# Optimization experiments

Measured on AMD Instinct MI355X. Metric: run time of the kernel, lower is better.

Reference implementation:

```python
import jax, jax.numpy as jnp
import numpy as np

B = 131072
D = 256
N_SC = 16
SC_CAP = 2
MAX_USERS = 8
POW_DIM = 10


def setup_inputs() -> dict:
    key = jax.random.key(0)
    k0, k1, k2, k3 = jax.random.split(key, 4)
    x = jax.random.normal(k0, (B, D), dtype=jnp.float32)
    available_actions = jax.random.randint(k1, (B, 2 * MAX_USERS), 0, 2).astype(jnp.int32)
    # per-head Categorical weights: Linear(D, action_dim), small init (gain=0.01 orthogonal-ish)
    W_sc = jax.random.normal(k2, (MAX_USERS, D, N_SC), dtype=jnp.float32) * 0.01
    b_sc = jnp.zeros((MAX_USERS, N_SC), dtype=jnp.float32)
    W_pow = jax.random.normal(k3, (MAX_USERS, D, POW_DIM), dtype=jnp.float32) * 0.01
    b_pow = jnp.zeros((MAX_USERS, POW_DIM), dtype=jnp.float32)
    return {"x": x, "available_actions": available_actions,
            "W_sc": W_sc, "b_sc": b_sc, "W_pow": W_pow, "b_pow": b_pow}


def reference(x, available_actions, W_sc, b_sc, W_pow, b_pow):
    # NOMA branch of MultiDiscreteACTLayer.forward (deterministic=False).
    Bn = x.shape[0]
    key = jax.random.key(42)
    sc_keys = jax.random.split(key, MAX_USERS)
    pow_key = jax.random.fold_in(key, 999)

    NEG = jnp.float32(-1e10)

    def sc_step(sc_stat, inp):
        W, b, avail, k = inp  # W:[D,N_SC], b:[N_SC], avail:[Bn] float, k: key
        logits = x @ W + b                       # [Bn, N_SC]
        mask = sc_stat < SC_CAP                  # subchannel still has capacity
        logits = jnp.where(mask, logits, NEG)
        action = jax.random.categorical(k, logits)        # [Bn] int
        logp = jnp.take_along_axis(jax.nn.log_softmax(logits, -1),
                                   action[:, None], axis=-1)[:, 0]
        # availability masking: unavailable -> action=-1, logp=0
        action = jnp.where(avail > 0, action, -1)
        logp = logp * avail
        # scatter: sc_stat[b, action] += 1 where action != -1
        upd = jnp.where((action >= 0)[:, None],
                        jax.nn.one_hot(jnp.maximum(action, 0), N_SC, dtype=sc_stat.dtype),
                        jnp.zeros((), sc_stat.dtype))
        return sc_stat + upd, (action, logp)

    sc_stat0 = jnp.zeros((Bn, N_SC), dtype=x.dtype)
    avail_f = available_actions.astype(x.dtype)
    avail_sc = avail_f[:, :MAX_USERS].T          # [MAX_USERS, Bn]
    _, (sc_actions, sc_logps) = jax.lax.scan(
        sc_step, sc_stat0, (W_sc, b_sc, avail_sc, sc_keys))

    # power heads: no mask, no loop-carried state -> fully batched
    pow_logits = jnp.einsum('bd,hdk->bhk', x, W_pow) + b_pow   # [Bn, H, POW_DIM]
    pow_actions = jax.random.categorical(pow_key, pow_logits)  # [Bn, H]
    pow_logps = jnp.take_along_axis(jax.nn.log_softmax(pow_logits, -1),
                                    pow_actions[..., None], axis=-1)[..., 0]
    avail_pow = avail_f[:, MAX_USERS:]
    pow_actions = jnp.where(avail_pow > 0, pow_actions, -1)
    pow_logps = pow_logps * avail_pow

    actions = jnp.concatenate([sc_actions.T, pow_actions], axis=-1)          # [Bn, 16]
    action_log_probs = jnp.concatenate([sc_logps.T, pow_logps], axis=-1)
    action_log_probs = jnp.sum(action_log_probs, axis=-1, keepdims=True)     # [Bn, 1]
    return actions, action_log_probs, available_actions
```

## Files before the change

### kernel.cpp

```cpp
#include <hip/hip_runtime.h>


#define B_TOTAL 131072
#define NCOL    208
#define ROWS    32
#define TINYF   1.17549435e-38f
#define THRF    2.0e-3f

#define WPLANE  53248
#define XB_L    8448
#define XB_P    264
#define LGP     36

typedef float f32x4 __attribute__((ext_vector_type(4)));
typedef short short8 __attribute__((ext_vector_type(8)));

#define MFMA_BF16(A,B,C) __builtin_amdgcn_mfma_f32_16x16x32_bf16((A),(B),(C),0,0,0)

#define ROR16(v, n) __uint_as_float((unsigned)__builtin_amdgcn_update_dpp(     \
    (int)__float_as_uint(v), (int)__float_as_uint(v), 0x120 | (n), 0xF, 0xF, false))

__device__ __forceinline__ float redmax16(float v) {
  v = fmaxf(v, ROR16(v, 8));
  v = fmaxf(v, ROR16(v, 4));
  v = fmaxf(v, ROR16(v, 2));
  v = fmaxf(v, ROR16(v, 1));
  return v;
}
__device__ __forceinline__ float redsum16(float v) {
  v += ROR16(v, 8);
  v += ROR16(v, 4);
  v += ROR16(v, 2);
  v += ROR16(v, 1);
  return v;
}

struct TF2 { unsigned a, b; };

__host__ __device__ constexpr unsigned rotl_(unsigned x, int r) {
  return (x << r) | (x >> (32 - r));
}

__host__ __device__ constexpr TF2 tf2(unsigned k0, unsigned k1, unsigned x0, unsigned x1) {
  unsigned ks0 = k0, ks1 = k1, ks2 = k0 ^ k1 ^ 0x1BD11BDAu;
  x0 += ks0; x1 += ks1;
  x0 += x1; x1 = rotl_(x1, 13); x1 ^= x0;
  x0 += x1; x1 = rotl_(x1, 15); x1 ^= x0;
  x0 += x1; x1 = rotl_(x1, 26); x1 ^= x0;
  x0 += x1; x1 = rotl_(x1,  6); x1 ^= x0;
  x0 += ks1; x1 += ks2 + 1u;
  x0 += x1; x1 = rotl_(x1, 17); x1 ^= x0;
  x0 += x1; x1 = rotl_(x1, 29); x1 ^= x0;
  x0 += x1; x1 = rotl_(x1, 16); x1 ^= x0;
  x0 += x1; x1 = rotl_(x1, 24); x1 ^= x0;
  x0 += ks2; x1 += ks0 + 2u;
  x0 += x1; x1 = rotl_(x1, 13); x1 ^= x0;
  x0 += x1; x1 = rotl_(x1, 15); x1 ^= x0;
  x0 += x1; x1 = rotl_(x1, 26); x1 ^= x0;
  x0 += x1; x1 = rotl_(x1,  6); x1 ^= x0;
  x0 += ks0; x1 += ks1 + 3u;
  x0 += x1; x1 = rotl_(x1, 17); x1 ^= x0;
  x0 += x1; x1 = rotl_(x1, 29); x1 ^= x0;
  x0 += x1; x1 = rotl_(x1, 16); x1 ^= x0;
  x0 += x1; x1 = rotl_(x1, 24); x1 ^= x0;
  x0 += ks1; x1 += ks2 + 4u;
  x0 += x1; x1 = rotl_(x1, 13); x1 ^= x0;
  x0 += x1; x1 = rotl_(x1, 15); x1 ^= x0;
  x0 += x1; x1 = rotl_(x1, 26); x1 ^= x0;
  x0 += x1; x1 = rotl_(x1,  6); x1 ^= x0;
  x0 += ks2; x1 += ks0 + 5u;
  return TF2{x0, x1};
}

__host__ __device__ constexpr unsigned key_a(unsigned d) { return tf2(0u, 42u, 0u, d).a; }
__host__ __device__ constexpr unsigned key_b(unsigned d) { return tf2(0u, 42u, 0u, d).b; }

constexpr unsigned SK0c[8] = {
  key_a(0), key_a(1), key_a(2), key_a(3), key_a(4), key_a(5), key_a(6), key_a(7)
};
constexpr unsigned SK1c[8] = {
  key_b(0), key_b(1), key_b(2), key_b(3), key_b(4), key_b(5), key_b(6), key_b(7)
};
constexpr unsigned PK0 = key_a(999);
constexpr unsigned PK1 = key_b(999);

__device__ __forceinline__ double dlog(double xd) {
  long long b = __double_as_longlong(xd);
  int e = (int)(b >> 52) - 1023;
  double m = __longlong_as_double((b & 0x000FFFFFFFFFFFFFLL) | 0x3FF0000000000000LL);
  if (m > 1.4142135623730951) { m *= 0.5; e += 1; }
  double mp1 = m + 1.0;
  double r = (double)__builtin_amdgcn_rcpf((float)mp1);
  r = fma(fma(-mp1, r, 1.0), r, r);
  double z  = (m - 1.0) * r;
  double z2 = z * z;
  double p = fma(z2, fma(z2, fma(z2, fma(z2, fma(z2,
              1.0/13.0, 1.0/11.0), 1.0/9.0), 1.0/7.0), 1.0/5.0), 1.0/3.0);
  double lm = fma(2.0 * z, z2 * p, 2.0 * z);
  return fma((double)e, 0.6931471805599453, lm);
}

__device__ __forceinline__ float gumbelf(unsigned bits) {
  float u = __uint_as_float((bits >> 9) | 0x3f800000u) - 1.0f;
  u = u + TINYF;
  u = fmaxf(TINYF, u);
  double nl = -dlog((double)u);
  return -(float)dlog(nl);
}

__device__ __attribute__((noinline)) float gumbel_precise(unsigned k0, unsigned k1,
                                                          unsigned cnt) {
  TF2 r = tf2(k0, k1, 0u, cnt);
  return gumbelf(r.a ^ r.b);
}

__device__ __forceinline__ float gumbel_fast(unsigned bits) {
  float u = __uint_as_float((bits >> 9) | 0x3f800000u) - 1.0f;
  u = fmaxf(TINYF, u + TINYF);
  float t = u - 1.0f;
  float q  = fmaf(t, 0.33333333f, -0.5f);
  float pl = -t * fmaf(t, q, 1.0f);
  float hw = -__logf(u);
  float nl = (t > -0.0078125f) ? pl : hw;
  return -__logf(nl);
}

__global__ void repack_kernel(const float* __restrict__ Wsc, const float* __restrict__ bsc,
                              const float* __restrict__ Wpow, const float* __restrict__ bpow,
                              short* __restrict__ Wb, float* __restrict__ bp) {
  int t = blockIdx.x * 256 + threadIdx.x;
  if (t < 53248) {
    int j    = t & 7;
    int lane = (t >> 3) & 63;
    int c    = (t >> 9) & 7;
    int T    = t >> 12;
    int k    = c * 32 + (lane >> 4) * 8 + j;
    int col  = T * 16 + (lane & 15);
    int u = col / 26, n = col % 26;
    float w = (n < 16) ? Wsc[(u * 256 + k) * 16 + n]
                       : Wpow[(u * 256 + k) * 10 + (n - 16)];
    unsigned b0 = __float_as_uint(w) & 0xFFFF0000u;
    float f1 = w - __uint_as_float(b0);
    unsigned b1 = __float_as_uint(f1) & 0xFFFF0000u;
    float f2 = f1 - __uint_as_float(b1);
    unsigned b2 = __float_as_uint(f2) & 0xFFFF0000u;
    int idx = (T * 8 + c) * 512 + lane * 8 + j;
    Wb[idx]              = (short)(b0 >> 16);
    Wb[WPLANE + idx]     = (short)(b1 >> 16);
    Wb[2 * WPLANE + idx] = (short)(b2 >> 16);
  } else {
    int cc = t - 53248;
    float v = 0.f;
    if (cc < NCOL) {
      int u = cc / 26, n = cc % 26;
      v = (n < 16) ? bsc[u * 16 + n] : bpow[u * 10 + (n - 16)];
    }
    bp[cc] = v;
  }
}

#define PROD8(X0, X1, X2, W0, W1, W2, AM, AS) do {                      \
    AM = MFMA_BF16(X0, W0, AM);                                         \
    AS = MFMA_BF16(X1, W0, AS);                                         \
    AS = MFMA_BF16(X0, W1, AS);                                         \
    AS = MFMA_BF16(X1, W1, AS);                                         \
    AS = MFMA_BF16(X2, W0, AS);                                         \
    AS = MFMA_BF16(X0, W2, AS);                                         \
    AS = MFMA_BF16(X2, W1, AS);                                         \
    AS = MFMA_BF16(X1, W2, AS);                                         \
  } while (0)

__global__ __launch_bounds__(512, 4) void act_kernel(
    const float* __restrict__ x, const int* __restrict__ avail,
    const short* __restrict__ Wb, const float* __restrict__ bp,
    float* __restrict__ out) {
  __shared__ __align__(16) union SMem {
    short xb[3][ROWS][XB_P];
    struct {
      float gpow[ROWS][80];
      float lgT[NCOL][LGP];
    } c;
  } sm;

  const int t = threadIdx.x;
  const int b0 = blockIdx.x * ROWS;

  const int av = avail[(size_t)(b0 + (t >> 4)) * 16 + (t & 15)];

#pragma unroll
  for (int i = 0; i < 4; ++i) {
    int flat = t + 512 * i;
    int r  = flat >> 6;
    int kq = flat & 63;
    float4 v = ((const float4*)(x + (size_t)(b0 + r) * 256))[kq];
    unsigned L0[4], L1[4], L2[4];
#pragma unroll
    for (int e = 0; e < 4; ++e) {
      float f = (&v.x)[e];
      unsigned h0 = __float_as_uint(f) & 0xFFFF0000u;
      float f1 = f - __uint_as_float(h0);
      unsigned h1 = __float_as_uint(f1) & 0xFFFF0000u;
      float f2 = f1 - __uint_as_float(h1);
      unsigned h2 = __float_as_uint(f2) & 0xFFFF0000u;
      L0[e] = h0; L1[e] = h1; L2[e] = h2;
    }
    int ks = 4 * kq;
    *(uint2*)&sm.xb[0][r][ks] =
        make_uint2((L0[0] >> 16) | (L0[1] & 0xFFFF0000u),
                   (L0[2] >> 16) | (L0[3] & 0xFFFF0000u));
    *(uint2*)&sm.xb[1][r][ks] =
        make_uint2((L1[0] >> 16) | (L1[1] & 0xFFFF0000u),
                   (L1[2] >> 16) | (L1[3] & 0xFFFF0000u));
    *(uint2*)&sm.xb[2][r][ks] =
        make_uint2((L2[0] >> 16) | (L2[1] & 0xFFFF0000u),
                   (L2[2] >> 16) | (L2[3] & 0xFFFF0000u));
  }
  __syncthreads();

  const int lane64 = t & 63;
  const int wv  = t >> 6;
  const int q   = lane64 >> 4;
  const int r16 = lane64 & 15;
  const int tA  = (wv + (blockIdx.x & 7)) & 7;
  const bool heavy = tA < 5;
  const int tB  = 8 + tA;

  const f32x4 fz = {0.f, 0.f, 0.f, 0.f};
  f32x4 dA0, dA1, dB0, dB1;
  int i0, jo;
  {
    f32x4 mA0 = fz, sA0 = fz, mA1 = fz, sA1 = fz;
    f32x4 mB0 = fz, sB0 = fz, mB1 = fz, sB1 = fz;

    const short* xr0 = &sm.xb[0][r16][0];
    const short* xr1 = &sm.xb[0][16 + r16][0];
    const int wlane = lane64 * 8;

#pragma unroll 1
    for (int c = 0; c < 8; ++c) {
      const int xo = c * 32 + q * 8;
      short8 a0 = *(const short8*)(xr0 + xo);
      short8 a1 = *(const short8*)(xr0 + XB_L + xo);
      short8 a2 = *(const short8*)(xr0 + 2 * XB_L + xo);
      short8 c0_ = *(const short8*)(xr1 + xo);
      short8 c1_ = *(const short8*)(xr1 + XB_L + xo);
      short8 c2_ = *(const short8*)(xr1 + 2 * XB_L + xo);
      {
        const int wi = (tA * 8 + c) * 512 + wlane;
        short8 w0 = *(const short8*)(Wb + wi);
        short8 w1 = *(const short8*)(Wb + WPLANE + wi);
        short8 w2 = *(const short8*)(Wb + 2 * WPLANE + wi);
        PROD8(a0,  a1,  a2,  w0, w1, w2, mA0, sA0);
        PROD8(c0_, c1_, c2_, w0, w1, w2, mA1, sA1);
      }
      if (heavy) {
        const int wi = (tB * 8 + c) * 512 + wlane;
        short8 w0 = *(const short8*)(Wb + wi);
        short8 w1 = *(const short8*)(Wb + WPLANE + wi);
        short8 w2 = *(const short8*)(Wb + 2 * WPLANE + wi);
        PROD8(a0,  a1,  a2,  w0, w1, w2, mB0, sB0);
        PROD8(c0_, c1_, c2_, w0, w1, w2, mB1, sB1);
      }
    }

    short8 pa = {0, 0, 0, 0, 0, 0, 0, 0};
    short8 pb = {0, 0, 0, 0, 0, 0, 0, 0};
    if (q == 0) {
      pa[0] = (short)(__float_as_uint((float)r16) >> 16);
      pb[0] = (short)0x3F80;
    }
    f32x4 pr = MFMA_BF16(pa, pb, fz);
    f32x4 pc = MFMA_BF16(pb, pa, fz);
    i0 = ((int)(pr[0] + 0.5f)) & 15;
    jo = ((int)(pc[0] + 0.5f)) & 15;

    dA0 = mA0 + sA0; dA1 = mA1 + sA1;
    dB0 = mB0 + sB0; dB1 = mB1 + sB1;
  }
  __syncthreads();

  {
    const int cA = tA * 16 + jo;
    float bpA = bp[cA];
    float4 v0, v1;
    v0.x = dA0[0] + bpA; v0.y = dA0[1] + bpA; v0.z = dA0[2] + bpA; v0.w = dA0[3] + bpA;
    v1.x = dA1[0] + bpA; v1.y = dA1[1] + bpA; v1.z = dA1[2] + bpA; v1.w = dA1[3] + bpA;
    *(float4*)&sm.c.lgT[cA][i0]      = v0;
    *(float4*)&sm.c.lgT[cA][16 + i0] = v1;
    if (heavy) {
      const int cB = tB * 16 + jo;
      float bpB = bp[cB];
      v0.x = dB0[0] + bpB; v0.y = dB0[1] + bpB; v0.z = dB0[2] + bpB; v0.w = dB0[3] + bpB;
      v1.x = dB1[0] + bpB; v1.y = dB1[1] + bpB; v1.z = dB1[2] + bpB; v1.w = dB1[3] + bpB;
      *(float4*)&sm.c.lgT[cB][i0]      = v0;
      *(float4*)&sm.c.lgT[cB][16 + i0] = v1;
    }
  }

#pragma unroll
  for (int i = 0; i < 5; ++i) {
    int flat = t + 512 * i;
    int prw  = (flat * 13108) >> 20;
    int q80  = flat - prw * 80;
    unsigned cnt = (unsigned)((b0 + prw) * 80 + q80);
    TF2 r = tf2(PK0, PK1, 0u, cnt);
    sm.c.gpow[prw][q80] = gumbel_fast(r.a ^ r.b);
  }

  float gsc[8];
  const unsigned cnt_sc = (unsigned)((b0 + (t >> 4)) * 16 + (t & 15));
#pragma unroll
  for (int u = 0; u < 8; ++u) {
    TF2 r = tf2(SK0c[u], SK1c[u], 0u, cnt_sc);
    gsc[u] = gumbel_fast(r.a ^ r.b);
  }
  __syncthreads();

  const int row  = t >> 4;
  const int lane = t & 15;
  const int g16  = (t & 63) >> 4;
  const int shamt = g16 * 16;
  const int gb   = b0 + row;
  const unsigned avm = (unsigned)((__ballot(av > 0) >> shamt) & 0xFFFFull);
  int stat = 0;
  float lpsum = 0.0f;
  float my_act = 0.0f;

#pragma unroll
  for (int u = 0; u < 8; ++u) {
    float logit = sm.c.lgT[u * 26 + lane][row];
    float ml = (stat < 2) ? logit : -1e10f;
    float y  = ml + gsc[u];
    float vmax = redmax16(y);
    unsigned bal = (unsigned)((__ballot(vmax - y < THRF) >> shamt) & 0xFFFFull);
    int idx;
    if (__builtin_popcount(bal) > 1) {
      float gp = gumbel_precise(SK0c[u], SK1c[u], cnt_sc);
      float yp = ml + gp;
      float vp = redmax16(yp);
      idx = __builtin_ctz((unsigned)((__ballot(yp == vp) >> shamt) & 0xFFFFull));
    } else {
      idx = __builtin_ctz(bal);
    }
    float s = redsum16(__expf(ml));
    float mlidx = redmax16((lane == idx) ? ml : -3.0e38f);
    float lp = mlidx - __logf(s);
    int au = (int)((avm >> u) & 1u);
    if (au) {
      lpsum += lp;
      if (lane == idx) stat += 1;
    }
    if (lane == u) my_act = au ? (float)idx : -1.0f;
  }

#pragma unroll
  for (int h = 0; h < 8; ++h) {
    bool on = lane < 10;
    float logit = on ? sm.c.lgT[h * 26 + 16 + lane][row] : -3.0e38f;
    float y     = on ? (logit + sm.c.gpow[row][h * 10 + lane]) : -3.0e38f;
    float vmax = redmax16(y);
    unsigned bal = (unsigned)((__ballot(vmax - y < THRF) >> shamt) & 0xFFFFull);
    int idx;
    if (__builtin_popcount(bal) > 1) {
      float gp = gumbel_precise(PK0, PK1, (unsigned)(gb * 80 + h * 10 + lane));
      float yp = on ? (logit + gp) : -3.0e38f;
      float vp = redmax16(yp);
      idx = __builtin_ctz((unsigned)((__ballot(yp == vp) >> shamt) & 0xFFFFull));
    } else {
      idx = __builtin_ctz(bal);
    }
    float s = redsum16(on ? __expf(logit) : 0.0f);
    float mlidx = redmax16((lane == idx) ? logit : -3.0e38f);
    float lp = mlidx - __logf(s);
    int ah = (int)((avm >> (8 + h)) & 1u);
    if (ah) lpsum += lp;
    if (lane == 8 + h) my_act = ah ? (float)idx : -1.0f;
  }

  out[(size_t)gb * 16 + lane] = my_act;
  if (lane == 0) out[(size_t)B_TOTAL * 16 + gb] = lpsum;
  out[(size_t)B_TOTAL * 17 + (size_t)gb * 16 + lane] = (float)av;
}

extern "C" void kernel_launch(void* const* d_in, const int* in_sizes, int n_in,
                              void* d_out, int out_size, void* d_ws, size_t ws_size,
                              hipStream_t stream) {
  const float* x    = (const float*)d_in[0];
  const int*   av   = (const int*)  d_in[1];
  const float* Wsc  = (const float*)d_in[2];
  const float* bsc  = (const float*)d_in[3];
  const float* Wpow = (const float*)d_in[4];
  const float* bpow = (const float*)d_in[5];
  float* outp = (float*)d_out;

  float* bp = (float*)d_ws;
  short* Wb = (short*)((char*)d_ws + 1024);

  repack_kernel<<<209, 256, 0, stream>>>(Wsc, bsc, Wpow, bpow, Wb, bp);
  act_kernel<<<B_TOTAL / ROWS, 512, 0, stream>>>(x, av, Wb, bp, outp);
}
```

Before: 361.8 us.

## Split fused kernel into GEMM and sampling kernels via global logits buffer

Splits the single fused kernel into a GEMM kernel that writes transposed logits to a workspace buffer and a separate sampling kernel that reads them back. The intent is to decouple the two phases so each gets its own block size and shared-memory footprint, improving occupancy. The cost is a large extra round trip of logits through global memory. The old fused kernel remains as a fallback when the workspace is too small.

```diff
diff --git a/kernel.cpp b/kernel.cpp
--- a/kernel.cpp
+++ b/kernel.cpp
@@ -170,6 +170,224 @@
     AS = MFMA_BF16(X1, W2, AS);                                         \
   } while (0)
 
+#define PHASE_A_BODY(XB, DA0, DA1, DB0, DB1, I0, JO)                          \
+  const int lane64 = t & 63;                                                  \
+  const int wv  = t >> 6;                                                     \
+  const int q   = lane64 >> 4;                                                \
+  const int r16 = lane64 & 15;                                                \
+  const int tA  = (wv + (blockIdx.x & 7)) & 7;                                \
+  const bool heavy = tA < 5;                                                  \
+  const int tB  = 8 + tA;                                                     \
+  const f32x4 fz = {0.f, 0.f, 0.f, 0.f};                                      \
+  {                                                                           \
+    f32x4 mA0 = fz, sA0 = fz, mA1 = fz, sA1 = fz;                             \
+    f32x4 mB0 = fz, sB0 = fz, mB1 = fz, sB1 = fz;                             \
+    const short* xr0 = &XB[0][r16][0];                                        \
+    const short* xr1 = &XB[0][16 + r16][0];                                   \
+    const int wlane = lane64 * 8;                                             \
+    _Pragma("unroll 1")                                                       \
+    for (int c = 0; c < 8; ++c) {                                             \
+      const int xo = c * 32 + q * 8;                                          \
+      short8 a0 = *(const short8*)(xr0 + xo);                                 \
+      short8 a1 = *(const short8*)(xr0 + XB_L + xo);                          \
+      short8 a2 = *(const short8*)(xr0 + 2 * XB_L + xo);                      \
+      short8 c0_ = *(const short8*)(xr1 + xo);                                \
+      short8 c1_ = *(const short8*)(xr1 + XB_L + xo);                         \
+      short8 c2_ = *(const short8*)(xr1 + 2 * XB_L + xo);                     \
+      {                                                                       \
+        const int wi = (tA * 8 + c) * 512 + wlane;                            \
+        short8 w0 = *(const short8*)(Wb + wi);                                \
+        short8 w1 = *(const short8*)(Wb + WPLANE + wi);                       \
+        short8 w2 = *(const short8*)(Wb + 2 * WPLANE + wi);                   \
+        PROD8(a0,  a1,  a2,  w0, w1, w2, mA0, sA0);                           \
+        PROD8(c0_, c1_, c2_, w0, w1, w2, mA1, sA1);                           \
+      }                                                                       \
+      if (heavy) {                                                            \
+        const int wi = (tB * 8 + c) * 512 + wlane;                            \
+        short8 w0 = *(const short8*)(Wb + wi);                                \
+        short8 w1 = *(const short8*)(Wb + WPLANE + wi);                       \
+        short8 w2 = *(const short8*)(Wb + 2 * WPLANE + wi);                   \
+        PROD8(a0,  a1,  a2,  w0, w1, w2, mB0, sB0);                           \
+        PROD8(c0_, c1_, c2_, w0, w1, w2, mB1, sB1);                           \
+      }                                                                       \
+    }                                                                         \
+    short8 pa = {0, 0, 0, 0, 0, 0, 0, 0};                                     \
+    short8 pb = {0, 0, 0, 0, 0, 0, 0, 0};                                     \
+    if (q == 0) {                                                             \
+      pa[0] = (short)(__float_as_uint((float)r16) >> 16);                     \
+      pb[0] = (short)0x3F80;                                                  \
+    }                                                                         \
+    f32x4 pr = MFMA_BF16(pa, pb, fz);                                         \
+    f32x4 pc = MFMA_BF16(pb, pa, fz);                                         \
+    I0 = ((int)(pr[0] + 0.5f)) & 15;                                          \
+    JO = ((int)(pc[0] + 0.5f)) & 15;                                          \
+    DA0 = mA0 + sA0; DA1 = mA1 + sA1;                                         \
+    DB0 = mB0 + sB0; DB1 = mB1 + sB1;                                         \
+  }
+
+#define STAGE_X(XB)                                                           \
+  _Pragma("unroll")                                                           \
+  for (int i = 0; i < 4; ++i) {                                               \
+    int flat = t + 512 * i;                                                   \
+    int r  = flat >> 6;                                                       \
+    int kq = flat & 63;                                                       \
+    float4 v = ((const float4*)(x + (size_t)(b0 + r) * 256))[kq];             \
+    unsigned L0[4], L1[4], L2[4];                                             \
+    _Pragma("unroll")                                                         \
+    for (int e = 0; e < 4; ++e) {                                             \
+      float f = (&v.x)[e];                                                    \
+      unsigned h0 = __float_as_uint(f) & 0xFFFF0000u;                         \
+      float f1 = f - __uint_as_float(h0);                                     \
+      unsigned h1 = __float_as_uint(f1) & 0xFFFF0000u;                        \
+      float f2 = f1 - __uint_as_float(h1);                                    \
+      unsigned h2 = __float_as_uint(f2) & 0xFFFF0000u;                        \
+      L0[e] = h0; L1[e] = h1; L2[e] = h2;                                     \
+    }                                                                         \
+    int ks = 4 * kq;                                                          \
+    *(uint2*)&XB[0][r][ks] =                                                  \
+        make_uint2((L0[0] >> 16) | (L0[1] & 0xFFFF0000u),                     \
+                   (L0[2] >> 16) | (L0[3] & 0xFFFF0000u));                    \
+    *(uint2*)&XB[1][r][ks] =                                                  \
+        make_uint2((L1[0] >> 16) | (L1[1] & 0xFFFF0000u),                     \
+                   (L1[2] >> 16) | (L1[3] & 0xFFFF0000u));                    \
+    *(uint2*)&XB[2][r][ks] =                                                  \
+        make_uint2((L2[0] >> 16) | (L2[1] & 0xFFFF0000u),                     \
+                   (L2[2] >> 16) | (L2[3] & 0xFFFF0000u));                    \
+  }
+
+__global__ __launch_bounds__(512, 4) void gemm_kernel(
+    const float* __restrict__ x, const short* __restrict__ Wb,
+    const float* __restrict__ bp, float* __restrict__ lgT) {
+  __shared__ __align__(16) short xb[3][ROWS][XB_P];
+  const int t = threadIdx.x;
+  const int b0 = blockIdx.x * ROWS;
+
+  STAGE_X(xb)
+  __syncthreads();
+
+  f32x4 dA0, dA1, dB0, dB1;
+  int i0, jo;
+  PHASE_A_BODY(xb, dA0, dA1, dB0, dB1, i0, jo)
+
+  {
+    const int cA = tA * 16 + jo;
+    float bpA = bp[cA];
+    float4 v0, v1;
+    v0.x = dA0[0] + bpA; v0.y = dA0[1] + bpA; v0.z = dA0[2] + bpA; v0.w = dA0[3] + bpA;
+    v1.x = dA1[0] + bpA; v1.y = dA1[1] + bpA; v1.z = dA1[2] + bpA; v1.w = dA1[3] + bpA;
+    float* base = lgT + (size_t)cA * B_TOTAL + b0;
+    *(float4*)(base + i0)      = v0;
+    *(float4*)(base + 16 + i0) = v1;
+    if (heavy) {
+      const int cB = tB * 16 + jo;
+      float bpB = bp[cB];
+      v0.x = dB0[0] + bpB; v0.y = dB0[1] + bpB; v0.z = dB0[2] + bpB; v0.w = dB0[3] + bpB;
+      v1.x = dB1[0] + bpB; v1.y = dB1[1] + bpB; v1.z = dB1[2] + bpB; v1.w = dB1[3] + bpB;
+      float* baseB = lgT + (size_t)cB * B_TOTAL + b0;
+      *(float4*)(baseB + i0)      = v0;
+      *(float4*)(baseB + 16 + i0) = v1;
+    }
+  }
+}
+
+__global__ __launch_bounds__(256, 4) void sample_kernel(
+    const float* __restrict__ lgT, const int* __restrict__ avail,
+    float* __restrict__ out) {
+  __shared__ float gpow[16][80];
+  const int t = threadIdx.x;
+  const int b0 = blockIdx.x * 16;
+  const int row  = t >> 4;
+  const int lane = t & 15;
+  const int gb   = b0 + row;
+  const int av = avail[(size_t)gb * 16 + lane];
+
+  float lsc[8];
+#pragma unroll
+  for (int u = 0; u < 8; ++u)
+    lsc[u] = lgT[(size_t)(u * 26 + lane) * B_TOTAL + gb];
+
+#pragma unroll
+  for (int i = 0; i < 5; ++i) {
+    int flat = t + 256 * i;
+    int prw  = (flat * 13108) >> 20;
+    int q80  = flat - prw * 80;
+    unsigned cnt = (unsigned)((b0 + prw) * 80 + q80);
+    TF2 r = tf2(PK0, PK1, 0u, cnt);
+    gpow[prw][q80] = gumbel_fast(r.a ^ r.b);
+  }
+
+  float gsc[8];
+  const unsigned cnt_sc = (unsigned)(gb * 16 + lane);
+#pragma unroll
+  for (int u = 0; u < 8; ++u) {
+    TF2 r = tf2(SK0c[u], SK1c[u], 0u, cnt_sc);
+    gsc[u] = gumbel_fast(r.a ^ r.b);
+  }
+  __syncthreads();
+
+  const int g16  = (t & 63) >> 4;
+  const int shamt = g16 * 16;
+  const unsigned avm = (unsigned)((__ballot(av > 0) >> shamt) & 0xFFFFull);
+  int stat = 0;
+  float lpsum = 0.0f;
+  float my_act = 0.0f;
+
+#pragma unroll
+  for (int u = 0; u < 8; ++u) {
+    float logit = lsc[u];
+    float ml = (stat < 2) ? logit : -1e10f;
+    float y  = ml + gsc[u];
+    float vmax = redmax16(y);
+    unsigned bal = (unsigned)((__ballot(vmax - y < THRF) >> shamt) & 0xFFFFull);
+    int idx;
+    if (__builtin_popcount(bal) > 1) {
+      float gp = gumbel_precise(SK0c[u], SK1c[u], cnt_sc);
+      float yp = ml + gp;
+      float vp = redmax16(yp);
+      idx = __builtin_ctz((unsigned)((__ballot(yp == vp) >> shamt) & 0xFFFFull));
+    } else {
+      idx = __builtin_ctz(bal);
+    }
+    float s = redsum16(__expf(ml));
+    float mlidx = redmax16((lane == idx) ? ml : -3.0e38f);
+    float lp = mlidx - __logf(s);
+    int au = (int)((avm >> u) & 1u);
+    if (au) {
+      lpsum += lp;
+      if (lane == idx) stat += 1;
+    }
+    if (lane == u) my_act = au ? (float)idx : -1.0f;
+  }
+
+#pragma unroll
+  for (int h = 0; h < 8; ++h) {
+    bool on = lane < 10;
+    float logit = on ? lgT[(size_t)(h * 26 + 16 + lane) * B_TOTAL + gb] : -3.0e38f;
+    float y     = on ? (logit + gpow[row][h * 10 + lane]) : -3.0e38f;
+    float vmax = redmax16(y);
+    unsigned bal = (unsigned)((__ballot(vmax - y < THRF) >> shamt) & 0xFFFFull);
+    int idx;
+    if (__builtin_popcount(bal) > 1) {
+      float gp = gumbel_precise(PK0, PK1, (unsigned)(gb * 80 + h * 10 + lane));
+      float yp = on ? (logit + gp) : -3.0e38f;
+      float vp = redmax16(yp);
+      idx = __builtin_ctz((unsigned)((__ballot(yp == vp) >> shamt) & 0xFFFFull));
+    } else {
+      idx = __builtin_ctz(bal);
+    }
+    float s = redsum16(on ? __expf(logit) : 0.0f);
+    float mlidx = redmax16((lane == idx) ? logit : -3.0e38f);
+    float lp = mlidx - __logf(s);
+    int ah = (int)((avm >> (8 + h)) & 1u);
+    if (ah) lpsum += lp;
+    if (lane == 8 + h) my_act = ah ? (float)idx : -1.0f;
+  }
+
+  out[(size_t)gb * 16 + lane] = my_act;
+  if (lane == 0) out[(size_t)B_TOTAL * 16 + gb] = lpsum;
+  out[(size_t)B_TOTAL * 17 + (size_t)gb * 16 + lane] = (float)av;
+}
+
 __global__ __launch_bounds__(512, 4) void act_kernel(
     const float* __restrict__ x, const int* __restrict__ avail,
     const short* __restrict__ Wb, const float* __restrict__ bp,
@@ -184,99 +402,14 @@
 
   const int t = threadIdx.x;
   const int b0 = blockIdx.x * ROWS;
-
   const int av = avail[(size_t)(b0 + (t >> 4)) * 16 + (t & 15)];
 
-#pragma unroll
-  for (int i = 0; i < 4; ++i) {
-    int flat = t + 512 * i;
-    int r  = flat >> 6;
-    int kq = flat & 63;
-    float4 v = ((const float4*)(x + (size_t)(b0 + r) * 256))[kq];
-    unsigned L0[4], L1[4], L2[4];
-#pragma unroll
-    for (int e = 0; e < 4; ++e) {
-      float f = (&v.x)[e];
-      unsigned h0 = __float_as_uint(f) & 0xFFFF0000u;
-      float f1 = f - __uint_as_float(h0);
-      unsigned h1 = __float_as_uint(f1) & 0xFFFF0000u;
-      float f2 = f1 - __uint_as_float(h1);
-      unsigned h2 = __float_as_uint(f2) & 0xFFFF0000u;
-      L0[e] = h0; L1[e] = h1; L2[e] = h2;
-    }
-    int ks = 4 * kq;
-    *(uint2*)&sm.xb[0][r][ks] =
-        make_uint2((L0[0] >> 16) | (L0[1] & 0xFFFF0000u),
-                   (L0[2] >> 16) | (L0[3] & 0xFFFF0000u));
-    *(uint2*)&sm.xb[1][r][ks] =
-        make_uint2((L1[0] >> 16) | (L1[1] & 0xFFFF0000u),
-                   (L1[2] >> 16) | (L1[3] & 0xFFFF0000u));
-    *(uint2*)&sm.xb[2][r][ks] =
-        make_uint2((L2[0] >> 16) | (L2[1] & 0xFFFF0000u),
-                   (L2[2] >> 16) | (L2[3] & 0xFFFF0000u));
-  }
+  STAGE_X(sm.xb)
   __syncthreads();
 
-  const int lane64 = t & 63;
-  const int wv  = t >> 6;
-  const int q   = lane64 >> 4;
-  const int r16 = lane64 & 15;
-  const int tA  = (wv + (blockIdx.x & 7)) & 7;
-  const bool heavy = tA < 5;
-  const int tB  = 8 + tA;
-
-  const f32x4 fz = {0.f, 0.f, 0.f, 0.f};
   f32x4 dA0, dA1, dB0, dB1;
   int i0, jo;
-  {
-    f32x4 mA0 = fz, sA0 = fz, mA1 = fz, sA1 = fz;
-    f32x4 mB0 = fz, sB0 = fz, mB1 = fz, sB1 = fz;
-
-    const short* xr0 = &sm.xb[0][r16][0];
-    const short* xr1 = &sm.xb[0][16 + r16][0];
-    const int wlane = lane64 * 8;
-
-#pragma unroll 1
-    for (int c = 0; c < 8; ++c) {
-      const int xo = c * 32 + q * 8;
-      short8 a0 = *(const short8*)(xr0 + xo);
-      short8 a1 = *(const short8*)(xr0 + XB_L + xo);
-      short8 a2 = *(const short8*)(xr0 + 2 * XB_L + xo);
-      short8 c0_ = *(const short8*)(xr1 + xo);
-      short8 c1_ = *(const short8*)(xr1 + XB_L + xo);
-      short8 c2_ = *(const short8*)(xr1 + 2 * XB_L + xo);
-      {
-        const int wi = (tA * 8 + c) * 512 + wlane;
-        short8 w0 = *(const short8*)(Wb + wi);
-        short8 w1 = *(const short8*)(Wb + WPLANE + wi);
-        short8 w2 = *(const short8*)(Wb + 2 * WPLANE + wi);
-        PROD8(a0,  a1,  a2,  w0, w1, w2, mA0, sA0);
-        PROD8(c0_, c1_, c2_, w0, w1, w2, mA1, sA1);
-      }
-      if (heavy) {
-        const int wi = (tB * 8 + c) * 512 + wlane;
-        short8 w0 = *(const short8*)(Wb + wi);
-        short8 w1 = *(const short8*)(Wb + WPLANE + wi);
-        short8 w2 = *(const short8*)(Wb + 2 * WPLANE + wi);
-        PROD8(a0,  a1,  a2,  w0, w1, w2, mB0, sB0);
-        PROD8(c0_, c1_, c2_, w0, w1, w2, mB1, sB1);
-      }
-    }
-
-    short8 pa = {0, 0, 0, 0, 0, 0, 0, 0};
-    short8 pb = {0, 0, 0, 0, 0, 0, 0, 0};
-    if (q == 0) {
-      pa[0] = (short)(__float_as_uint((float)r16) >> 16);
-      pb[0] = (short)0x3F80;
-    }
-    f32x4 pr = MFMA_BF16(pa, pb, fz);
-    f32x4 pc = MFMA_BF16(pb, pa, fz);
-    i0 = ((int)(pr[0] + 0.5f)) & 15;
-    jo = ((int)(pc[0] + 0.5f)) & 15;
-
-    dA0 = mA0 + sA0; dA1 = mA1 + sA1;
-    dB0 = mB0 + sB0; dB1 = mB1 + sB1;
-  }
+  PHASE_A_BODY(sm.xb, dA0, dA1, dB0, dB1, i0, jo)
   __syncthreads();
 
   {
@@ -395,7 +528,15 @@
 
   float* bp = (float*)d_ws;
   short* Wb = (short*)((char*)d_ws + 1024);
+  const size_t lgoff = 1024 + (size_t)3 * WPLANE * sizeof(short);
+  float* lgT = (float*)((char*)d_ws + lgoff);
+  const size_t need = lgoff + (size_t)NCOL * B_TOTAL * sizeof(float);
 
   repack_kernel<<<209, 256, 0, stream>>>(Wsc, bsc, Wpow, bpow, Wb, bp);
-  act_kernel<<<B_TOTAL / ROWS, 512, 0, stream>>>(x, av, Wb, bp, outp);
-}
+  if (ws_size >= need) {
+    gemm_kernel<<<B_TOTAL / ROWS, 512, 0, stream>>>(x, Wb, bp, lgT);
+    sample_kernel<<<B_TOTAL / 16, 256, 0, stream>>>(lgT, av, outp);
+  } else {
+    act_kernel<<<B_TOTAL / ROWS, 512, 0, stream>>>(x, av, Wb, bp, outp);
+  }
+}
```

Result: slower. 379.4 us (+4.9%).
